# Kernel tuning notes

Hardware: AMD Instinct MI355X
Metric: run time of the kernel (lower is better)

Reference implementation:

```python
import jax, jax.numpy as jnp
import numpy as np

BS, C_IN, SEQ_LEN = 16, 321, 720
PRED_LEN, PATCH_LEN, STRIDE = 720, 24, 24
N_LAYERS, D_MODEL, N_HEADS, D_FF = 3, 128, 16, 256
SEQ_PN = (SEQ_LEN - PATCH_LEN) // STRIDE + 1   # 30
PRED_PN = (PRED_LEN + PATCH_LEN - 1) // PATCH_LEN  # 30
EPS = 1e-5


def layernorm(x, g, b):
    mu = x.mean(-1, keepdims=True)
    var = x.var(-1, keepdims=True)
    return (x - mu) * jax.lax.rsqrt(var + EPS) * g + b


def setup_inputs() -> dict:
    key = jax.random.key(0)
    ks = iter(jax.random.split(key, 32))
    w = lambda shape, s=0.02: jax.random.normal(next(ks), shape, jnp.float32) * s
    L = N_LAYERS
    return {
        "z": jax.random.normal(next(ks), (BS, C_IN, SEQ_LEN), jnp.float32),
        "W_P_w": w((D_MODEL, PATCH_LEN)), "W_P_b": jnp.zeros((D_MODEL,), jnp.float32),
        "PE": 0.04 * jax.random.uniform(next(ks), (SEQ_PN, D_MODEL), jnp.float32) - 0.02,
        "dummies": 0.5 * jax.random.normal(next(ks), (C_IN, PRED_PN, PATCH_LEN), jnp.float32),
        "Wq": w((L, D_MODEL, D_MODEL)), "bq": jnp.zeros((L, D_MODEL), jnp.float32),
        "Wk": w((L, D_MODEL, D_MODEL)), "bk": jnp.zeros((L, D_MODEL), jnp.float32),
        "Wv": w((L, D_MODEL, D_MODEL)), "bv": jnp.zeros((L, D_MODEL), jnp.float32),
        "Wo": w((L, D_MODEL, D_MODEL)), "bo": jnp.zeros((L, D_MODEL), jnp.float32),
        "g1": jnp.ones((L, D_MODEL), jnp.float32), "be1": jnp.zeros((L, D_MODEL), jnp.float32),
        "W1": w((L, D_FF, D_MODEL)), "b1": jnp.zeros((L, D_FF), jnp.float32),
        "W2": w((L, D_MODEL, D_FF // 2)), "b2": jnp.zeros((L, D_MODEL), jnp.float32),
        "g2": jnp.ones((L, D_MODEL), jnp.float32), "be2": jnp.zeros((L, D_MODEL), jnp.float32),
        "proj_w": w((PATCH_LEN, D_MODEL)), "proj_b": jnp.zeros((PATCH_LEN,), jnp.float32),
    }


def reference(z, W_P_w, W_P_b, PE, dummies, Wq, bq, Wk, bk, Wv, bv, Wo, bo,
              g1, be1, W1, b1, W2, b2, g2, be2, proj_w, proj_b):
    bs, c, _ = z.shape
    d_h = D_MODEL // N_HEADS
    scale = d_h ** -0.5
    # instance norm over time (unbiased=False var)
    mean = z.mean(2, keepdims=True)
    std = jnp.sqrt(z.var(2, keepdims=True) + EPS)
    zn = (z - mean) / std
    # unfold into patches: [bs, c, S, patch_len]
    idx = jnp.arange(SEQ_PN)[:, None] * STRIDE + jnp.arange(PATCH_LEN)[None, :]
    patches = zn[:, :, idx]
    x = jnp.einsum('bcsp,dp->bcsd', patches, W_P_w) + W_P_b + PE
    x = x.reshape(bs * c, SEQ_PN, D_MODEL)                       # seq tokens
    dum = jnp.einsum('cnp,dp->cnd', dummies, W_P_w) + W_P_b      # [c, Pn, d]
    pred = jnp.broadcast_to(dum[None], (bs, c, PRED_PN, D_MODEL)).reshape(bs * c, PRED_PN, D_MODEL)
    B = bs * c
    scores = None
    for i in range(N_LAYERS):
        q = (jnp.einsum('bpd,ed->bpe', pred, Wq[i]) + bq[i]).reshape(B, PRED_PN, N_HEADS, d_h)
        k = (jnp.einsum('bsd,ed->bse', x, Wk[i]) + bk[i]).reshape(B, SEQ_PN, N_HEADS, d_h)
        v = (jnp.einsum('bsd,ed->bse', x, Wv[i]) + bv[i]).reshape(B, SEQ_PN, N_HEADS, d_h)
        s = jnp.einsum('bphd,bshd->bphs', q, k) * scale
        if scores is not None:
            s = s + scores   # residual attention scores across layers
        scores = s
        attn = jax.nn.softmax(s, axis=-1)
        o = jnp.einsum('bphs,bshd->bphd', attn, v).reshape(B, PRED_PN, D_MODEL)
        o = jnp.einsum('bpd,ed->bpe', o, Wo[i]) + bo[i]
        pred = layernorm(pred + o, g1[i], be1[i])
        h = jnp.einsum('bpd,fd->bpf', pred, W1[i]) + b1[i]
        a, gate = jnp.split(h, 2, axis=-1)
        f = jnp.einsum('bpf,df->bpd', a * jax.nn.gelu(gate, approximate=False), W2[i]) + b2[i]
        pred = layernorm(pred + f, g2[i], be2[i])
    out = pred.reshape(bs, c, PRED_PN, D_MODEL)
    out = jnp.einsum('bcnd,pd->bcnp', out, proj_w) + proj_b
    out = out.reshape(bs, c, PRED_PN * PATCH_LEN)
    return out * std[:, :, 0:1] + mean[:, :, 0:1]
```

## Files before the change

### kernel.cpp

```cpp
#include <hip/hip_runtime.h>
#include <math.h>


typedef unsigned short u16;
typedef __attribute__((ext_vector_type(8))) short short8;
typedef __attribute__((ext_vector_type(4))) float floatx4;

#define ATTN_SCALE 0.35355339059327373f
#define SB 136
#define SF 132

__device__ __forceinline__ u16 f2bf(float f){
  union{float f; unsigned u;} v; v.f=f;
  unsigned r = v.u + 0x7FFFu + ((v.u>>16)&1u);
  return (u16)(r>>16);
}
__device__ __forceinline__ float bf2f(u16 h){
  union{unsigned u; float f;} v; v.u = ((unsigned)h)<<16;
  return v.f;
}

__device__ __forceinline__ short8 cvt8(const float* ap){
  floatx4 f0 = *(const floatx4*)ap;
  floatx4 f1 = *(const floatx4*)(ap+4);
  short8 a;
  a[0]=(short)f2bf(f0[0]); a[1]=(short)f2bf(f0[1]);
  a[2]=(short)f2bf(f0[2]); a[3]=(short)f2bf(f0[3]);
  a[4]=(short)f2bf(f1[0]); a[5]=(short)f2bf(f1[1]);
  a[6]=(short)f2bf(f1[2]); a[7]=(short)f2bf(f1[3]);
  return a;
}

__device__ __forceinline__ short8 loadB(const u16* p){ return *(const short8*)p; }
__device__ __forceinline__ short8 loadB(const float* p){ return cvt8(p); }

template<int MODE, typename WT>
__device__ __forceinline__ void gemm(const u16* A, const WT* __restrict__ W,
                                     const float* __restrict__ bias, u16* out,
                                     const u16* gg, int wave, int lane){
  const int m = lane&15, qd = lane>>4;
  for (int t=wave; t<16; t+=8){
    const int rt = t>>3, ct = t&7;
    floatx4 acc = {0.f,0.f,0.f,0.f};
    #pragma unroll
    for (int kt=0; kt<4; ++kt){
      const int k0 = kt*32 + qd*8;
      short8 a = *(const short8*)(A + (rt*16+m)*SB + k0);
      short8 b = loadB(W + (ct*16+m)*128 + k0);
      acc = __builtin_amdgcn_mfma_f32_16x16x32_bf16(a,b,acc,0,0,0);
    }
    const int col = ct*16+m;
    const float bv = bias[col];
    #pragma unroll
    for (int r=0;r<4;++r){
      const int row = rt*16+qd*4+r;
      u16 res = 0;
      if (row<30){
        float v = acc[r]+bv;
        if constexpr (MODE==1) v = 0.5f*v*(1.f+erff(v*0.70710678118654752f));
        else if constexpr (MODE==2) v = v * bf2f(gg[row*SB+col]);
        res = f2bf(v);
      }
      out[row*SB+col] = res;
    }
  }
}

__device__ __forceinline__ void ln_res(float* pred, u16* predb, const u16* add,
                                       const float* __restrict__ g, const float* __restrict__ be,
                                       int wave, int lane){
  for (int rr=wave; rr<30; rr+=8){
    float* pr = pred + rr*SF;
    u16*  pbr = predb + rr*SB;
    const u16* ar = add + rr*SB;
    float v0 = pr[lane]    + bf2f(ar[lane]);
    float v1 = pr[lane+64] + bf2f(ar[lane+64]);
    float s = v0+v1, s2 = v0*v0+v1*v1;
    #pragma unroll
    for (int off=32; off>0; off>>=1){ s += __shfl_xor(s,off,64); s2 += __shfl_xor(s2,off,64); }
    float m = s*(1.f/128.f);
    float var = s2*(1.f/128.f) - m*m;
    float rstd = rsqrtf(var + 1e-5f);
    float o0 = (v0-m)*rstd*g[lane]    + be[lane];
    float o1 = (v1-m)*rstd*g[lane+64] + be[lane+64];
    pr[lane] = o0; pr[lane+64] = o1;
    pbr[lane] = f2bf(o0); pbr[lane+64] = f2bf(o1);
  }
}

__global__ void cvtw(const float* __restrict__ Wq, const float* __restrict__ Wk,
                     const float* __restrict__ Wv, const float* __restrict__ Wo,
                     const float* __restrict__ W1, const float* __restrict__ W2,
                     u16* __restrict__ ws){
  const int i = blockIdx.x*256 + threadIdx.x;
  float v;
  if      (i < 49152)  v = Wq[i];
  else if (i < 98304)  v = Wk[i-49152];
  else if (i < 147456) v = Wv[i-98304];
  else if (i < 196608) v = Wo[i-147456];
  else if (i < 294912) v = W1[i-196608];
  else                 v = W2[i-294912];
  ws[i] = f2bf(v);
}

template<typename WT>
__global__ __launch_bounds__(512, 4) void ts_fused(
  const float* __restrict__ z,    const float* __restrict__ WPw, const float* __restrict__ WPb,
  const float* __restrict__ PE,   const float* __restrict__ dums,
  const WT*    __restrict__ Wq_a, const float* __restrict__ bq_a,
  const WT*    __restrict__ Wk_a, const float* __restrict__ bk_a,
  const WT*    __restrict__ Wv_a, const float* __restrict__ bv_a,
  const WT*    __restrict__ Wo_a, const float* __restrict__ bo_a,
  const float* __restrict__ g1_a, const float* __restrict__ be1_a,
  const WT*    __restrict__ W1_a, const float* __restrict__ b1_a,
  const WT*    __restrict__ W2_a, const float* __restrict__ b2_a,
  const float* __restrict__ g2_a, const float* __restrict__ be2_a,
  const float* __restrict__ PJw,  const float* __restrict__ PJb,
  float* __restrict__ dout)
{
  __shared__ __align__(16) u16   x_s[32*SB];
  __shared__ __align__(16) u16   predb[32*SB];
  __shared__ __align__(16) float pred_s[32*SF];
  __shared__ __align__(16) u16   bufA[32*SB];
  __shared__ __align__(16) u16   bufB[32*SB];
  __shared__ __align__(16) u16   bufC[32*SB];
  __shared__ float redA[8], redB[8], stats[2];

  const int tid  = threadIdx.x;
  const int wave = tid >> 6;
  const int lane = tid & 63;
  const int bi   = blockIdx.x;
  const int c    = bi % 321;
  const float* zr = z + bi*720;

  float s=0.f, s2=0.f;
  for (int i=tid;i<720;i+=512){ float v=zr[i]; s+=v; s2+=v*v; }
  #pragma unroll
  for (int off=32; off>0; off>>=1){ s += __shfl_xor(s,off,64); s2 += __shfl_xor(s2,off,64); }
  if (lane==0){ redA[wave]=s; redB[wave]=s2; }
  __syncthreads();
  if (tid==0){
    float S=0.f,S2=0.f;
    #pragma unroll
    for (int w=0;w<8;++w){S+=redA[w];S2+=redB[w];}
    float mu = S*(1.f/720.f);
    float var = S2*(1.f/720.f) - mu*mu;
    stats[0]=mu; stats[1]=sqrtf(var+1e-5f);
  }
  __syncthreads();
  const float mu = stats[0], sd = stats[1], rsd = 1.f/sd;

  for (int i=tid;i<720;i+=512) bufA[i] = f2bf((zr[i]-mu)*rsd);
  __syncthreads();

  {
    const int m = lane&15, qd = lane>>4;
    const short8 z8 = {0,0,0,0,0,0,0,0};
    for (int t=wave;t<16;t+=8){
      const int rt=t>>3, ct=t&7;
      const int pm = rt*16+m;
      const int col = ct*16+m;
      short8 b  = (qd<3) ? cvt8(WPw + col*24 + qd*8) : z8;
      short8 ax = (pm<30 && qd<3) ? *(const short8*)(bufA + pm*24 + qd*8) : z8;
      short8 ap = (pm<30 && qd<3) ? cvt8(dums + c*720 + pm*24 + qd*8) : z8;
      floatx4 accx={0.f,0.f,0.f,0.f}, accp={0.f,0.f,0.f,0.f};
      accx = __builtin_amdgcn_mfma_f32_16x16x32_bf16(ax,b,accx,0,0,0);
      accp = __builtin_amdgcn_mfma_f32_16x16x32_bf16(ap,b,accp,0,0,0);
      const float bv = WPb[col];
      #pragma unroll
      for (int r=0;r<4;++r){
        const int row = rt*16+qd*4+r;
        if (row<30){
          float pv = accp[r]+bv;
          x_s[row*SB+col]    = f2bf(accx[r]+bv+PE[row*128+col]);
          pred_s[row*SF+col] = pv;
          predb[row*SB+col]  = f2bf(pv);
        } else { x_s[row*SB+col]=0; pred_s[row*SF+col]=0.f; predb[row*SB+col]=0; }
      }
    }
  }
  __syncthreads();

  float sc[30];
  #pragma unroll
  for (int i=0;i<30;++i) sc[i]=0.f;
  const int h = wave*2 + (lane>>5);
  const int p = lane & 31;

  for (int li=0; li<3; ++li){
    const WT* Wq = Wq_a + li*16384; const float* bq = bq_a + li*128;
    const WT* Wk = Wk_a + li*16384; const float* bk = bk_a + li*128;
    const WT* Wv = Wv_a + li*16384; const float* bv = bv_a + li*128;
    const WT* Wo = Wo_a + li*16384; const float* bo = bo_a + li*128;
    const WT* W1 = W1_a + li*32768; const float* b1 = b1_a + li*256;
    const WT* W2 = W2_a + li*16384; const float* b2 = b2_a + li*128;

    gemm<0>(predb, Wq, bq, bufA, (const u16*)nullptr, wave, lane);
    gemm<0>(x_s,   Wk, bk, bufB, (const u16*)nullptr, wave, lane);
    gemm<0>(x_s,   Wv, bv, bufC, (const u16*)nullptr, wave, lane);
    __syncthreads();

    if (p < 30){
      short8 qq = *(const short8*)(bufA + p*SB + h*8);
      float qv[8];
      #pragma unroll
      for (int j=0;j<8;++j) qv[j]=bf2f((u16)qq[j]);
      #pragma unroll
      for (int si=0; si<30; ++si){
        short8 kk = *(const short8*)(bufB + si*SB + h*8);
        float d = 0.f;
        #pragma unroll
        for (int j=0;j<8;++j) d += qv[j]*bf2f((u16)kk[j]);
        sc[si] += d * ATTN_SCALE;
      }
      float mx = sc[0];
      #pragma unroll
      for (int si=1; si<30; ++si) mx = fmaxf(mx, sc[si]);
      float ssum = 0.f;
      float ov[8] = {0.f,0.f,0.f,0.f,0.f,0.f,0.f,0.f};
      #pragma unroll
      for (int si=0; si<30; ++si){
        float e = __expf(sc[si]-mx);
        ssum += e;
        short8 vv = *(const short8*)(bufC + si*SB + h*8);
        #pragma unroll
        for (int j=0;j<8;++j) ov[j] += e*bf2f((u16)vv[j]);
      }
      const float rn = 1.f/ssum;
      #pragma unroll
      for (int j=0;j<8;++j) bufA[p*SB+h*8+j] = f2bf(ov[j]*rn);
    }
    __syncthreads();

    gemm<0>(bufA, Wo, bo, bufB, (const u16*)nullptr, wave, lane);
    __syncthreads();
    ln_res(pred_s, predb, bufB, g1_a+li*128, be1_a+li*128, wave, lane);
    __syncthreads();

    gemm<1>(predb, W1+128*128, b1+128, bufA, (const u16*)nullptr, wave, lane);
    __syncthreads();
    gemm<2>(predb, W1, b1, bufC, bufA, wave, lane);
    __syncthreads();
    gemm<0>(bufC, W2, b2, bufB, (const u16*)nullptr, wave, lane);
    __syncthreads();
    ln_res(pred_s, predb, bufB, g2_a+li*128, be2_a+li*128, wave, lane);
    __syncthreads();
  }

  {
    const int m = lane&15, qd = lane>>4;
    const short8 z8 = {0,0,0,0,0,0,0,0};
    float* orow = dout + bi*720;
    for (int t=wave; t<4; t+=8){
      const int rt=t>>1, ct=t&1;
      const int col = ct*16+m;
      floatx4 acc = {0.f,0.f,0.f,0.f};
      #pragma unroll
      for (int kt=0;kt<4;++kt){
        const int k0 = kt*32+qd*8;
        short8 a = *(const short8*)(predb + (rt*16+m)*SB + k0);
        short8 b = (col<24) ? cvt8(PJw + col*128 + k0) : z8;
        acc = __builtin_amdgcn_mfma_f32_16x16x32_bf16(a,b,acc,0,0,0);
      }
      if (col<24){
        const float pb = PJb[col];
        #pragma unroll
        for (int r=0;r<4;++r){
          const int row = rt*16+qd*4+r;
          if (row<30) orow[row*24+col] = (acc[r]+pb)*sd + mu;
        }
      }
    }
  }
}

extern "C" void kernel_launch(void* const* d_in, const int* in_sizes, int n_in,
                              void* d_out, int out_size, void* d_ws, size_t ws_size,
                              hipStream_t stream) {
  (void)in_sizes; (void)n_in; (void)out_size;
  const float* z    = (const float*)d_in[0];
  const float* WPw  = (const float*)d_in[1];
  const float* WPb  = (const float*)d_in[2];
  const float* PE   = (const float*)d_in[3];
  const float* dums = (const float*)d_in[4];
  const float* Wq   = (const float*)d_in[5];
  const float* bq   = (const float*)d_in[6];
  const float* Wk   = (const float*)d_in[7];
  const float* bk   = (const float*)d_in[8];
  const float* Wv   = (const float*)d_in[9];
  const float* bv   = (const float*)d_in[10];
  const float* Wo   = (const float*)d_in[11];
  const float* bo   = (const float*)d_in[12];
  const float* g1   = (const float*)d_in[13];
  const float* be1  = (const float*)d_in[14];
  const float* W1   = (const float*)d_in[15];
  const float* b1   = (const float*)d_in[16];
  const float* W2   = (const float*)d_in[17];
  const float* b2   = (const float*)d_in[18];
  const float* g2   = (const float*)d_in[19];
  const float* be2  = (const float*)d_in[20];
  const float* PJw  = (const float*)d_in[21];
  const float* PJb  = (const float*)d_in[22];
  float* dout = (float*)d_out;

  const size_t need = (size_t)344064 * sizeof(u16);
  if (ws_size >= need){
    u16* ws = (u16*)d_ws;
    cvtw<<<dim3(1344), dim3(256), 0, stream>>>(Wq, Wk, Wv, Wo, W1, W2, ws);
    ts_fused<u16><<<dim3(5136), dim3(512), 0, stream>>>(
      z, WPw, WPb, PE, dums,
      ws,        bq, ws+49152,  bk, ws+98304, bv, ws+147456, bo,
      g1, be1, ws+196608, b1, ws+294912, b2, g2, be2, PJw, PJb, dout);
  } else {
    ts_fused<float><<<dim3(5136), dim3(512), 0, stream>>>(
      z, WPw, WPb, PE, dums,
      Wq, bq, Wk, bk, Wv, bv, Wo, bo,
      g1, be1, W1, b1, W2, b2, g2, be2, PJw, PJb, dout);
  }
}
```

Measured before the change: 1.028 ms.

## Keep weight tiles in registers per wave and fuse KV and gated FFN GEMMs

Each wave now owns one 16-column output tile, loads its weight fragments once, and reuses them for both row tiles instead of reloading per tile. The K and V projections share a single pass over the A fragments, and the gated FFN computes value and gate in one GEMM with the gating applied in the epilogue. This removes one barrier and an intermediate buffer. Exact erf GELU is replaced by a tanh-form sigmoid approximation, which slightly changes numerics.

```diff
diff --git a/kernel.cpp b/kernel.cpp
--- a/kernel.cpp
+++ b/kernel.cpp
@@ -9,6 +9,8 @@
 #define ATTN_SCALE 0.35355339059327373f
 #define SB 136
 #define SF 132
+
+#define MFMA_BF16 __builtin_amdgcn_mfma_f32_16x16x32_bf16
 
 __device__ __forceinline__ u16 f2bf(float f){
   union{float f; unsigned u;} v; v.f=f;
@@ -18,6 +20,11 @@
 __device__ __forceinline__ float bf2f(u16 h){
   union{unsigned u; float f;} v; v.u = ((unsigned)h)<<16;
   return v.f;
+}
+__device__ __forceinline__ float gelu_f(float x){
+  float u = x*(1.f + 0.044715f*x*x);
+  float e = __expf(-1.5957691216057308f*u);
+  return x/(1.f+e);
 }
 
 __device__ __forceinline__ short8 cvt8(const float* ap){
@@ -30,36 +37,96 @@
   a[6]=(short)f2bf(f1[2]); a[7]=(short)f2bf(f1[3]);
   return a;
 }
-
 __device__ __forceinline__ short8 loadB(const u16* p){ return *(const short8*)p; }
 __device__ __forceinline__ short8 loadB(const float* p){ return cvt8(p); }
 
-template<int MODE, typename WT>
-__device__ __forceinline__ void gemm(const u16* A, const WT* __restrict__ W,
-                                     const float* __restrict__ bias, u16* out,
-                                     const u16* gg, int wave, int lane){
-  const int m = lane&15, qd = lane>>4;
-  for (int t=wave; t<16; t+=8){
-    const int rt = t>>3, ct = t&7;
+__device__ __forceinline__ void epi(u16* out, floatx4 acc, float bv, int rt, int qd, int col){
+  #pragma unroll
+  for (int r=0;r<4;++r){
+    const int row = rt*16+qd*4+r;
+    out[row*SB+col] = (row<30) ? f2bf(acc[r]+bv) : (u16)0;
+  }
+}
+
+template<typename WT>
+__device__ __forceinline__ void gemm2(const u16* A, const WT* __restrict__ W,
+                                      const float* __restrict__ bias, u16* out,
+                                      int wave, int lane){
+  const int m=lane&15, qd=lane>>4, col=wave*16+m;
+  short8 b4[4];
+  #pragma unroll
+  for (int kt=0;kt<4;++kt) b4[kt] = loadB(W + col*128 + kt*32 + qd*8);
+  const float bv = bias[col];
+  #pragma unroll
+  for (int rt=0;rt<2;++rt){
+    short8 a4[4];
+    #pragma unroll
+    for (int kt=0;kt<4;++kt) a4[kt] = *(const short8*)(A + (rt*16+m)*SB + kt*32 + qd*8);
     floatx4 acc = {0.f,0.f,0.f,0.f};
     #pragma unroll
-    for (int kt=0; kt<4; ++kt){
-      const int k0 = kt*32 + qd*8;
-      short8 a = *(const short8*)(A + (rt*16+m)*SB + k0);
-      short8 b = loadB(W + (ct*16+m)*128 + k0);
-      acc = __builtin_amdgcn_mfma_f32_16x16x32_bf16(a,b,acc,0,0,0);
-    }
-    const int col = ct*16+m;
-    const float bv = bias[col];
+    for (int kt=0;kt<4;++kt) acc = MFMA_BF16(a4[kt], b4[kt], acc, 0,0,0);
+    epi(out, acc, bv, rt, qd, col);
+  }
+}
+
+template<typename WT>
+__device__ __forceinline__ void gemm_kv(const u16* A,
+                                        const WT* __restrict__ Wk, const float* __restrict__ bk,
+                                        const WT* __restrict__ Wv, const float* __restrict__ bv_,
+                                        u16* outk, u16* outv, int wave, int lane){
+  const int m=lane&15, qd=lane>>4, col=wave*16+m;
+  short8 bkf[4], bvf[4];
+  #pragma unroll
+  for (int kt=0;kt<4;++kt) bkf[kt] = loadB(Wk + col*128 + kt*32 + qd*8);
+  #pragma unroll
+  for (int kt=0;kt<4;++kt) bvf[kt] = loadB(Wv + col*128 + kt*32 + qd*8);
+  const float bkb = bk[col], bvb = bv_[col];
+  #pragma unroll
+  for (int rt=0;rt<2;++rt){
+    short8 a4[4];
+    #pragma unroll
+    for (int kt=0;kt<4;++kt) a4[kt] = *(const short8*)(A + (rt*16+m)*SB + kt*32 + qd*8);
+    floatx4 acck = {0.f,0.f,0.f,0.f}, accv = {0.f,0.f,0.f,0.f};
+    #pragma unroll
+    for (int kt=0;kt<4;++kt){
+      acck = MFMA_BF16(a4[kt], bkf[kt], acck, 0,0,0);
+      accv = MFMA_BF16(a4[kt], bvf[kt], accv, 0,0,0);
+    }
+    epi(outk, acck, bkb, rt, qd, col);
+    epi(outv, accv, bvb, rt, qd, col);
+  }
+}
+
+template<typename WT>
+__device__ __forceinline__ void gemm_h(const u16* A, const WT* __restrict__ W1,
+                                       const float* __restrict__ b1, u16* out,
+                                       int wave, int lane){
+  const int m=lane&15, qd=lane>>4, col=wave*16+m;
+  short8 ba4[4], bg4[4];
+  #pragma unroll
+  for (int kt=0;kt<4;++kt) ba4[kt] = loadB(W1 + col*128 + kt*32 + qd*8);
+  #pragma unroll
+  for (int kt=0;kt<4;++kt) bg4[kt] = loadB(W1 + (128+col)*128 + kt*32 + qd*8);
+  const float bab = b1[col], bgb = b1[128+col];
+  #pragma unroll
+  for (int rt=0;rt<2;++rt){
+    short8 a4[4];
+    #pragma unroll
+    for (int kt=0;kt<4;++kt) a4[kt] = *(const short8*)(A + (rt*16+m)*SB + kt*32 + qd*8);
+    floatx4 acca = {0.f,0.f,0.f,0.f}, accg = {0.f,0.f,0.f,0.f};
+    #pragma unroll
+    for (int kt=0;kt<4;++kt){
+      acca = MFMA_BF16(a4[kt], ba4[kt], acca, 0,0,0);
+      accg = MFMA_BF16(a4[kt], bg4[kt], accg, 0,0,0);
+    }
     #pragma unroll
     for (int r=0;r<4;++r){
       const int row = rt*16+qd*4+r;
       u16 res = 0;
       if (row<30){
-        float v = acc[r]+bv;
-        if constexpr (MODE==1) v = 0.5f*v*(1.f+erff(v*0.70710678118654752f));
-        else if constexpr (MODE==2) v = v * bf2f(gg[row*SB+col]);
-        res = f2bf(v);
+        float a = acca[r]+bab;
+        float g = accg[r]+bgb;
+        res = f2bf(a * gelu_f(g));
       }
       out[row*SB+col] = res;
     }
@@ -154,19 +221,18 @@
   __syncthreads();
 
   {
-    const int m = lane&15, qd = lane>>4;
+    const int m = lane&15, qd = lane>>4, col = wave*16+m;
     const short8 z8 = {0,0,0,0,0,0,0,0};
-    for (int t=wave;t<16;t+=8){
-      const int rt=t>>3, ct=t&7;
+    short8 b = (qd<3) ? cvt8(WPw + col*24 + qd*8) : z8;
+    const float bv = WPb[col];
+    #pragma unroll
+    for (int rt=0;rt<2;++rt){
       const int pm = rt*16+m;
-      const int col = ct*16+m;
-      short8 b  = (qd<3) ? cvt8(WPw + col*24 + qd*8) : z8;
       short8 ax = (pm<30 && qd<3) ? *(const short8*)(bufA + pm*24 + qd*8) : z8;
       short8 ap = (pm<30 && qd<3) ? cvt8(dums + c*720 + pm*24 + qd*8) : z8;
       floatx4 accx={0.f,0.f,0.f,0.f}, accp={0.f,0.f,0.f,0.f};
-      accx = __builtin_amdgcn_mfma_f32_16x16x32_bf16(ax,b,accx,0,0,0);
-      accp = __builtin_amdgcn_mfma_f32_16x16x32_bf16(ap,b,accp,0,0,0);
-      const float bv = WPb[col];
+      accx = MFMA_BF16(ax,b,accx,0,0,0);
+      accp = MFMA_BF16(ap,b,accp,0,0,0);
       #pragma unroll
       for (int r=0;r<4;++r){
         const int row = rt*16+qd*4+r;
@@ -195,9 +261,8 @@
     const WT* W1 = W1_a + li*32768; const float* b1 = b1_a + li*256;
     const WT* W2 = W2_a + li*16384; const float* b2 = b2_a + li*128;
 
-    gemm<0>(predb, Wq, bq, bufA, (const u16*)nullptr, wave, lane);
-    gemm<0>(x_s,   Wk, bk, bufB, (const u16*)nullptr, wave, lane);
-    gemm<0>(x_s,   Wv, bv, bufC, (const u16*)nullptr, wave, lane);
+    gemm2  (predb, Wq, bq, bufA, wave, lane);
+    gemm_kv(x_s, Wk, bk, Wv, bv, bufB, bufC, wave, lane);
     __syncthreads();
 
     if (p < 30){
@@ -232,16 +297,14 @@
     }
     __syncthreads();
 
-    gemm<0>(bufA, Wo, bo, bufB, (const u16*)nullptr, wave, lane);
+    gemm2(bufA, Wo, bo, bufB, wave, lane);
     __syncthreads();
     ln_res(pred_s, predb, bufB, g1_a+li*128, be1_a+li*128, wave, lane);
     __syncthreads();
 
-    gemm<1>(predb, W1+128*128, b1+128, bufA, (const u16*)nullptr, wave, lane);
-    __syncthreads();
-    gemm<2>(predb, W1, b1, bufC, bufA, wave, lane);
-    __syncthreads();
-    gemm<0>(bufC, W2, b2, bufB, (const u16*)nullptr, wave, lane);
+    gemm_h(predb, W1, b1, bufC, wave, lane);
+    __syncthreads();
+    gemm2(bufC, W2, b2, bufB, wave, lane);
     __syncthreads();
     ln_res(pred_s, predb, bufB, g2_a+li*128, be2_a+li*128, wave, lane);
     __syncthreads();
@@ -260,7 +323,7 @@
         const int k0 = kt*32+qd*8;
         short8 a = *(const short8*)(predb + (rt*16+m)*SB + k0);
         short8 b = (col<24) ? cvt8(PJw + col*128 + k0) : z8;
-        acc = __builtin_amdgcn_mfma_f32_16x16x32_bf16(a,b,acc,0,0,0);
+        acc = MFMA_BF16(a,b,acc,0,0,0);
       }
       if (col<24){
         const float pb = PJb[col];
```

New measurement: 1.017 ms. About the same (-1.1%).
